# Performance work log

Hardware: AMD Instinct MI355X
Metric: run time of the kernel (lower is better)

The kernel has to match this reference:

```python
import jax, jax.numpy as jnp
import numpy as np

EPS = 1e-16

def _householder_cascade(vectors):
    # vectors: [N, S, 1]
    v = vectors[..., 0]                                  # [N, S]
    outer = jnp.einsum('ns,nt->nst', v, v)               # [N, S, S]
    inner = jnp.sum(v * v, axis=-1)[:, None, None]       # [N, 1, 1]
    S = v.shape[-1]
    I = jnp.eye(S, dtype=vectors.dtype)
    hh = I[None] - 2.0 * outer / (inner + EPS)           # [N, S, S]
    # sequential left-to-right product: Q = H_0 @ H_1 @ ... @ H_{N-1}
    def step(Q, M):
        return Q @ M, None
    Q, _ = jax.lax.scan(step, I, hh)
    return Q

def setup_inputs() -> dict:
    key = jax.random.key(0)
    k1, k2 = jax.random.split(key)
    S, N, B = 256, 258, 65536
    vectors = jax.random.normal(k1, (N, S, 1), dtype=jnp.float32)
    vectors = vectors / jnp.linalg.norm(vectors, axis=1, keepdims=True)
    x = jax.random.normal(k2, (B, S), dtype=jnp.float32)
    return {"x": x, "vectors": vectors}

def reference(x, vectors):
    Q = _householder_cascade(vectors)   # [S, S]
    return x @ Q.T
```

## Files before the change

### kernel.cpp

```cpp
#include <hip/hip_runtime.h>


#define GLOAD_LDS16(g, l)                                                      \
  __builtin_amdgcn_global_load_lds(                                            \
      (const __attribute__((address_space(1))) void*)(g),                      \
      (__attribute__((address_space(3))) void*)(l), 16, 0, 0)

typedef __attribute__((ext_vector_type(8))) short bf16x8;
typedef __attribute__((ext_vector_type(4))) float f32x4;

__device__ __forceinline__ unsigned short f2bf_rne(float f) {
  unsigned u = __builtin_bit_cast(unsigned, f);
  return (unsigned short)((u + 0x7fffu + ((u >> 16) & 1u)) >> 16);
}

struct bfpair { short hi, lo; };

__device__ __forceinline__ bfpair bf_split(float x) {
  unsigned short hu = f2bf_rne(x);
  float hf = __builtin_bit_cast(float, (unsigned)hu << 16);
  bfpair r;
  r.hi = (short)hu;
  r.lo = (short)f2bf_rne(x - hf);
  return r;
}

template <int CTRL>
__device__ __forceinline__ float dpp_add(float v) {
  int t = __builtin_amdgcn_update_dpp(0, __builtin_bit_cast(int, v), CTRL, 0xF,
                                      0xF, true);
  return v + __builtin_bit_cast(float, t);
}

__global__ void hh_scale(const float* __restrict__ vecs, float* __restrict__ u) {
  const int n = blockIdx.x;
  const int l = threadIdx.x;
  float4* uo = (float4*)(u + (long)n * 256) + l;
  if (n >= 258) {
    *uo = make_float4(0.f, 0.f, 0.f, 0.f);
    return;
  }
  const float4 v = *((const float4*)(vecs + (long)n * 256) + l);
  float p = v.x * v.x + v.y * v.y + v.z * v.z + v.w * v.w;
#pragma unroll
  for (int off = 32; off; off >>= 1) p += __shfl_xor(p, off);
  const float s = sqrtf(2.0f / (p + 1e-16f));
  *uo = make_float4(v.x * s, v.y * s, v.z * s, v.w * s);
}

__launch_bounds__(64, 1)
__global__ void hh_qchunk(const float* __restrict__ u,
                          float* __restrict__ Qc) {
  const int l = threadIdx.x;
  const int chunk = blockIdx.x >> 6;
  const int rg = blockIdx.x & 63;
  const int r = l >> 4;
  const int c = l & 15;
  const int row = rg * 4 + r;
  const int col0 = c * 16;

  float q[16];
#pragma unroll
  for (int i = 0; i < 16; ++i) q[i] = (col0 + i == row) ? 1.f : 0.f;

  const float* ub = u + (long)chunk * 33 * 256 + col0;

  auto load16 = [&](float(&d)[16], int n) {
    const float4* v = (const float4*)(ub + (long)n * 256);
#pragma unroll
    for (int i = 0; i < 4; ++i) {
      float4 t = v[i];
      d[4 * i] = t.x; d[4 * i + 1] = t.y; d[4 * i + 2] = t.z; d[4 * i + 3] = t.w;
    }
  };

  auto step = [&](const float(&a)[16]) {
    float p0 = 0.f, p1 = 0.f, p2 = 0.f, p3 = 0.f;
#pragma unroll
    for (int e = 0; e < 4; ++e) {
      p0 = fmaf(q[e], a[e], p0);
      p1 = fmaf(q[4 + e], a[4 + e], p1);
      p2 = fmaf(q[8 + e], a[8 + e], p2);
      p3 = fmaf(q[12 + e], a[12 + e], p3);
    }
    float p = (p0 + p1) + (p2 + p3);
    p = dpp_add<0xB1>(p);
    p = dpp_add<0x4E>(p);
    p = dpp_add<0x124>(p);
    p = dpp_add<0x128>(p);
#pragma unroll
    for (int k = 0; k < 16; ++k) q[k] = fmaf(-p, a[k], q[k]);
  };

  float A0[16], A1[16];
  load16(A0, 0);
  load16(A1, 1);
  for (int n = 0; n < 32; n += 2) {
    step(A0);
    load16(A0, n + 2);
    step(A1);
    load16(A1, n + 3);
  }
  step(A0);

  float4* out = (float4*)(Qc + (long)chunk * 65536 + row * 256 + col0);
#pragma unroll
  for (int i = 0; i < 4; ++i)
    out[i] = make_float4(q[4 * i], q[4 * i + 1], q[4 * i + 2], q[4 * i + 3]);
}

__launch_bounds__(256)
__global__ void hh_merge(const float* __restrict__ in, float* __restrict__ out,
                         unsigned short* __restrict__ outb, int to_bf16) {
  const int b = blockIdx.x >> 4;
  const int t = blockIdx.x & 15;
  const int bi = (t >> 2) * 64, bj = (t & 3) * 64;
  const int tid = threadIdx.x;
  const int lane = tid & 63, wid = tid >> 6;
  const int wm = wid >> 1, wn = wid & 1;
  const int fr = lane & 15, fg = lane >> 4;
  const float* A = in + (long)b * 2 * 65536;
  const float* Bm = A + 65536;

  const int ar0 = bi + wm * 32;
  const int bc0 = bj + wn * 32;

  f32x4 acc[2][2];
#pragma unroll
  for (int m = 0; m < 2; ++m)
#pragma unroll
    for (int n = 0; n < 2; ++n) acc[m][n] = (f32x4){0.f, 0.f, 0.f, 0.f};

  for (int kt = 0; kt < 8; ++kt) {
    const int k0 = kt * 32 + fg * 8;
    bf16x8 ahi[2], alo[2], bhi[2], blo[2];
#pragma unroll
    for (int m = 0; m < 2; ++m) {
      const float* ap = A + (long)(ar0 + m * 16 + fr) * 256 + k0;
      f32x4 x0 = *(const f32x4*)ap;
      f32x4 x1 = *(const f32x4*)(ap + 4);
#pragma unroll
      for (int e = 0; e < 4; ++e) {
        bfpair p0 = bf_split(x0[e]);
        bfpair p1 = bf_split(x1[e]);
        ahi[m][e] = p0.hi; alo[m][e] = p0.lo;
        ahi[m][4 + e] = p1.hi; alo[m][4 + e] = p1.lo;
      }
    }
#pragma unroll
    for (int n = 0; n < 2; ++n) {
      const float* bp = Bm + (long)k0 * 256 + bc0 + n * 16 + fr;
#pragma unroll
      for (int e = 0; e < 8; ++e) {
        bfpair pb = bf_split(bp[e * 256]);
        bhi[n][e] = pb.hi; blo[n][e] = pb.lo;
      }
    }
#pragma unroll
    for (int m = 0; m < 2; ++m)
#pragma unroll
      for (int n = 0; n < 2; ++n) {
        acc[m][n] = __builtin_amdgcn_mfma_f32_16x16x32_bf16(ahi[m], bhi[n],
                                                            acc[m][n], 0, 0, 0);
        acc[m][n] = __builtin_amdgcn_mfma_f32_16x16x32_bf16(ahi[m], blo[n],
                                                            acc[m][n], 0, 0, 0);
        acc[m][n] = __builtin_amdgcn_mfma_f32_16x16x32_bf16(alo[m], bhi[n],
                                                            acc[m][n], 0, 0, 0);
      }
  }

#pragma unroll
  for (int m = 0; m < 2; ++m)
#pragma unroll
    for (int n = 0; n < 2; ++n)
#pragma unroll
      for (int rr = 0; rr < 4; ++rr) {
        const int grow = ar0 + m * 16 + fg * 4 + rr;
        const int gcol = bc0 + n * 16 + fr;
        if (to_bf16)
          outb[(long)b * 65536 + grow * 256 + gcol] = f2bf_rne(acc[m][n][rr]);
        else
          out[(long)b * 65536 + grow * 256 + gcol] = acc[m][n][rr];
      }
}

__launch_bounds__(512)
__global__ void hh_gemm(const float* __restrict__ X,
                        const unsigned short* __restrict__ Qb,
                        float* __restrict__ Y) {
  __shared__ __align__(128) char lds[65536];
  const int tid = threadIdx.x;
  const int lane = tid & 63;
  const int wid = tid >> 6;
  const int wm = wid >> 2;
  const int wn = wid & 3;
  const int fr = lane & 15;
  const int fg = lane >> 4;
  const long bm0 = (long)blockIdx.x * 128;

  auto stage = [&](int buf, int kt) {
#pragma unroll
    for (int r2 = 0; r2 < 2; ++r2) {
      int slot = r2 * 512 + tid;
      int row = slot >> 3, seg = slot & 7;
      int ps = seg ^ (row & 7);
      GLOAD_LDS16(X + (bm0 + row) * 256 + kt * 32 + ps * 4,
                  lds + buf * 16384 + slot * 16);
    }
#pragma unroll
    for (int r2 = 0; r2 < 2; ++r2) {
      int slot = r2 * 512 + tid;
      int row = slot >> 2, seg = slot & 3;
      int ps = seg ^ (row & 3);
      GLOAD_LDS16(Qb + row * 256 + kt * 32 + ps * 8,
                  lds + 32768 + buf * 16384 + slot * 16);
    }
  };

  f32x4 acc[4][4];
#pragma unroll
  for (int m = 0; m < 4; ++m)
#pragma unroll
    for (int n = 0; n < 4; ++n) acc[m][n] = (f32x4){0.f, 0.f, 0.f, 0.f};

  stage(0, 0);
  __syncthreads();

  for (int kt = 0; kt < 8; ++kt) {
    const int cur = kt & 1;
    if (kt < 7) stage(cur ^ 1, kt + 1);

    bf16x8 aF[4], bF[4];
#pragma unroll
    for (int m = 0; m < 4; ++m) {
      int row = wm * 64 + m * 16 + fr;
      int s0 = (2 * fg) ^ (row & 7);
      int s1 = (2 * fg + 1) ^ (row & 7);
      const f32x4 x0 = *(const f32x4*)(lds + cur * 16384 + row * 128 + s0 * 16);
      const f32x4 x1 = *(const f32x4*)(lds + cur * 16384 + row * 128 + s1 * 16);
      bf16x8 t;
      t[0] = (short)f2bf_rne(x0[0]);
      t[1] = (short)f2bf_rne(x0[1]);
      t[2] = (short)f2bf_rne(x0[2]);
      t[3] = (short)f2bf_rne(x0[3]);
      t[4] = (short)f2bf_rne(x1[0]);
      t[5] = (short)f2bf_rne(x1[1]);
      t[6] = (short)f2bf_rne(x1[2]);
      t[7] = (short)f2bf_rne(x1[3]);
      aF[m] = t;
    }
#pragma unroll
    for (int n = 0; n < 4; ++n) {
      int row = wn * 64 + n * 16 + fr;
      int ps = fg ^ (row & 3);
      bF[n] = *(const bf16x8*)(lds + 32768 + cur * 16384 + row * 64 + ps * 16);
    }
#pragma unroll
    for (int m = 0; m < 4; ++m)
#pragma unroll
      for (int n = 0; n < 4; ++n)
        acc[m][n] =
            __builtin_amdgcn_mfma_f32_16x16x32_bf16(aF[m], bF[n], acc[m][n], 0, 0, 0);
    __syncthreads();
  }

#pragma unroll
  for (int m = 0; m < 4; ++m)
#pragma unroll
    for (int n = 0; n < 4; ++n)
#pragma unroll
      for (int r = 0; r < 4; ++r) {
        long grow = bm0 + wm * 64 + m * 16 + fg * 4 + r;
        int gcol = wn * 64 + n * 16 + fr;
        Y[grow * 256 + gcol] = acc[m][n][r];
      }
}

extern "C" void kernel_launch(void* const* d_in, const int* in_sizes, int n_in,
                              void* d_out, int out_size, void* d_ws, size_t ws_size,
                              hipStream_t stream) {
  const float* x = (const float*)d_in[0];
  const float* vecs = (const float*)d_in[1];
  float* y = (float*)d_out;

  char* ws = (char*)d_ws;
  float* u = (float*)ws;
  unsigned short* Qb = (unsigned short*)(ws + 278528);

  char* ob = (char*)d_out;
  float* Qc = (float*)(ob);
  float* P = (float*)(ob + 2097152);
  float* R = (float*)(ob + 3145728);

  hh_scale<<<272, 64, 0, stream>>>(vecs, u);
  hh_qchunk<<<512, 64, 0, stream>>>(u, Qc);
  hh_merge<<<64, 256, 0, stream>>>(Qc, P, nullptr, 0);
  hh_merge<<<32, 256, 0, stream>>>(P, R, nullptr, 0);
  hh_merge<<<16, 256, 0, stream>>>(R, nullptr, Qb, 1);
  hh_gemm<<<512, 512, 0, stream>>>(x, Qb, y);
}
```

Measured before the change: 75.66 us.

## Store transposed Q chunks so merge loads B contiguously, use smaller merge blocks

Each Q chunk product is now written in both row-major and transposed form. The merge GEMM can then read B operands as contiguous float4 rows instead of strided scalar column reads. Merge blocks shrink from four waves on 64x64 tiles to one wave on 32x32 tiles, which launches more blocks for the small merge tree and so uses more CUs. In exchange every stage writes twice as much data, including scattered strided transposed stores, and uses more scratch space in the output buffer.

```diff
diff --git a/kernel.cpp b/kernel.cpp
--- a/kernel.cpp
+++ b/kernel.cpp
@@ -50,7 +50,8 @@
 
 __launch_bounds__(64, 1)
 __global__ void hh_qchunk(const float* __restrict__ u,
-                          float* __restrict__ Qc) {
+                          float* __restrict__ Qc,
+                          float* __restrict__ QcT) {
   const int l = threadIdx.x;
   const int chunk = blockIdx.x >> 6;
   const int rg = blockIdx.x & 63;
@@ -107,23 +108,23 @@
 #pragma unroll
   for (int i = 0; i < 4; ++i)
     out[i] = make_float4(q[4 * i], q[4 * i + 1], q[4 * i + 2], q[4 * i + 3]);
-}
-
-__launch_bounds__(256)
-__global__ void hh_merge(const float* __restrict__ in, float* __restrict__ out,
+  float* outT = QcT + (long)chunk * 65536 + row;
+#pragma unroll
+  for (int i = 0; i < 16; ++i) outT[(col0 + i) * 256] = q[i];
+}
+
+__launch_bounds__(64)
+__global__ void hh_merge(const float* __restrict__ A0,
+                         const float* __restrict__ BT0,
+                         float* __restrict__ C0, float* __restrict__ CT0,
                          unsigned short* __restrict__ outb, int to_bf16) {
-  const int b = blockIdx.x >> 4;
-  const int t = blockIdx.x & 15;
-  const int bi = (t >> 2) * 64, bj = (t & 3) * 64;
-  const int tid = threadIdx.x;
-  const int lane = tid & 63, wid = tid >> 6;
-  const int wm = wid >> 1, wn = wid & 1;
+  const int p = blockIdx.x >> 6;
+  const int t = blockIdx.x & 63;
+  const int ti = (t >> 3) * 32, tj = (t & 7) * 32;
+  const int lane = threadIdx.x;
   const int fr = lane & 15, fg = lane >> 4;
-  const float* A = in + (long)b * 2 * 65536;
-  const float* Bm = A + 65536;
-
-  const int ar0 = bi + wm * 32;
-  const int bc0 = bj + wn * 32;
+  const float* A = A0 + (long)p * 2 * 65536;
+  const float* BT = BT0 + (long)p * 2 * 65536 + 65536;
 
   f32x4 acc[2][2];
 #pragma unroll
@@ -136,7 +137,7 @@
     bf16x8 ahi[2], alo[2], bhi[2], blo[2];
 #pragma unroll
     for (int m = 0; m < 2; ++m) {
-      const float* ap = A + (long)(ar0 + m * 16 + fr) * 256 + k0;
+      const float* ap = A + (long)(ti + m * 16 + fr) * 256 + k0;
       f32x4 x0 = *(const f32x4*)ap;
       f32x4 x1 = *(const f32x4*)(ap + 4);
 #pragma unroll
@@ -149,11 +150,15 @@
     }
 #pragma unroll
     for (int n = 0; n < 2; ++n) {
-      const float* bp = Bm + (long)k0 * 256 + bc0 + n * 16 + fr;
-#pragma unroll
-      for (int e = 0; e < 8; ++e) {
-        bfpair pb = bf_split(bp[e * 256]);
-        bhi[n][e] = pb.hi; blo[n][e] = pb.lo;
+      const float* bp = BT + (long)(tj + n * 16 + fr) * 256 + k0;
+      f32x4 x0 = *(const f32x4*)bp;
+      f32x4 x1 = *(const f32x4*)(bp + 4);
+#pragma unroll
+      for (int e = 0; e < 4; ++e) {
+        bfpair p0 = bf_split(x0[e]);
+        bfpair p1 = bf_split(x1[e]);
+        bhi[n][e] = p0.hi; blo[n][e] = p0.lo;
+        bhi[n][4 + e] = p1.hi; blo[n][4 + e] = p1.lo;
       }
     }
 #pragma unroll
@@ -175,12 +180,15 @@
     for (int n = 0; n < 2; ++n)
 #pragma unroll
       for (int rr = 0; rr < 4; ++rr) {
-        const int grow = ar0 + m * 16 + fg * 4 + rr;
-        const int gcol = bc0 + n * 16 + fr;
-        if (to_bf16)
-          outb[(long)b * 65536 + grow * 256 + gcol] = f2bf_rne(acc[m][n][rr]);
-        else
-          out[(long)b * 65536 + grow * 256 + gcol] = acc[m][n][rr];
+        const int grow = ti + m * 16 + fg * 4 + rr;
+        const int gcol = tj + n * 16 + fr;
+        const float val = acc[m][n][rr];
+        if (to_bf16) {
+          outb[grow * 256 + gcol] = f2bf_rne(val);
+        } else {
+          C0[(long)p * 65536 + grow * 256 + gcol] = val;
+          CT0[(long)p * 65536 + gcol * 256 + grow] = val;
+        }
       }
 }
 
@@ -288,14 +296,17 @@
   unsigned short* Qb = (unsigned short*)(ws + 278528);
 
   char* ob = (char*)d_out;
-  float* Qc = (float*)(ob);
-  float* P = (float*)(ob + 2097152);
-  float* R = (float*)(ob + 3145728);
+  float* Qc  = (float*)(ob);
+  float* QcT = (float*)(ob + 2097152);
+  float* P   = (float*)(ob + 4194304);
+  float* PT  = (float*)(ob + 5242880);
+  float* R   = (float*)(ob + 6291456);
+  float* RT  = (float*)(ob + 6815744);
 
   hh_scale<<<272, 64, 0, stream>>>(vecs, u);
-  hh_qchunk<<<512, 64, 0, stream>>>(u, Qc);
-  hh_merge<<<64, 256, 0, stream>>>(Qc, P, nullptr, 0);
-  hh_merge<<<32, 256, 0, stream>>>(P, R, nullptr, 0);
-  hh_merge<<<16, 256, 0, stream>>>(R, nullptr, Qb, 1);
+  hh_qchunk<<<512, 64, 0, stream>>>(u, Qc, QcT);
+  hh_merge<<<256, 64, 0, stream>>>(Qc, QcT, P, PT, nullptr, 0);
+  hh_merge<<<128, 64, 0, stream>>>(P, PT, R, RT, nullptr, 0);
+  hh_merge<<<64, 64, 0, stream>>>(R, RT, nullptr, nullptr, Qb, 1);
   hh_gemm<<<512, 512, 0, stream>>>(x, Qb, y);
 }
```

After: 71.09 us, median of 2. 6.0% less time.
